# Performance work log

Measured on AMD Instinct MI355X. Metric: run time of the kernel, lower is better.

## Reference

```python
import jax, jax.numpy as jnp
import numpy as np

B, S, D, H = 4, 2048, 2048, 16
HD = D // H  # head_dim = 128


def setup_inputs() -> dict:
    key = jax.random.key(0)
    ks = jax.random.split(key, 9)
    s = 1.0 / np.sqrt(D)
    return {
        "x": jax.random.normal(ks[0], (B, S, D), dtype=jnp.float32),
        "wq": jax.random.normal(ks[1], (D, D), dtype=jnp.float32) * s,
        "bq": jnp.zeros((D,), dtype=jnp.float32),
        "wk": jax.random.normal(ks[2], (D, D), dtype=jnp.float32) * s,
        "bk": jnp.zeros((D,), dtype=jnp.float32),
        "wv": jax.random.normal(ks[3], (D, D), dtype=jnp.float32) * s,
        "bv": jnp.zeros((D,), dtype=jnp.float32),
        "wo": jax.random.normal(ks[4], (D, D), dtype=jnp.float32) * s,
        "bo": jnp.zeros((D,), dtype=jnp.float32),
    }


def reference(x, wq, bq, wk, bk, wv, bv, wo, bo):
    scale = HD ** -0.5
    # projections: [B,S,D] -> [B,S,H,HD] -> [B,H,S,HD]
    def split_heads(t):
        return t.reshape(B, S, H, HD).transpose(0, 2, 1, 3)
    q = split_heads(x @ wq + bq)
    k = split_heads(x @ wk + bk)
    v = split_heads(x @ wv + bv)
    scores = jnp.einsum('bhqd,bhkd->bhqk', q, k) * scale  # [B,H,S,S]
    attn = jax.nn.softmax(scores, axis=-1)
    out = jnp.einsum('bhqk,bhkd->bhqd', attn, v)  # [B,H,S,HD]
    out = out.transpose(0, 2, 1, 3).reshape(B, S, D)
    return out @ wo + bo
```

## Files before the change

kernel.cpp:

```cpp
#include <hip/hip_runtime.h>
#include <hip/hip_bf16.h>


typedef __attribute__((ext_vector_type(8))) short short8;
typedef __attribute__((ext_vector_type(4))) float floatx4;

#define DEV __device__ __forceinline__

DEV short f2bf(float f) {
    __hip_bfloat16 h = __float2bfloat16(f);
    return *reinterpret_cast<short*>(&h);
}

DEV void load_lds16(const __hip_bfloat16* g, short* l) {
    __builtin_amdgcn_global_load_lds(
        (const __attribute__((address_space(1))) void*)g,
        (__attribute__((address_space(3))) void*)l, 16, 0, 0);
}

__global__ void cast_x_kernel(const float* __restrict__ in,
                              __hip_bfloat16* __restrict__ out, int n8) {
    int i = blockIdx.x * 256 + threadIdx.x;
    if (i >= n8) return;
    const float4* p = reinterpret_cast<const float4*>(in) + (size_t)i * 2;
    float4 a = p[0], b = p[1];
    short8 r;
    r[0] = f2bf(a.x); r[1] = f2bf(a.y); r[2] = f2bf(a.z); r[3] = f2bf(a.w);
    r[4] = f2bf(b.x); r[5] = f2bf(b.y); r[6] = f2bf(b.z); r[7] = f2bf(b.w);
    *reinterpret_cast<short8*>(reinterpret_cast<short*>(out) + (size_t)i * 8) = r;
}

__global__ void transpose_cast_kernel(const float* __restrict__ wq,
                                      const float* __restrict__ wk,
                                      const float* __restrict__ wv,
                                      const float* __restrict__ wo,
                                      short* __restrict__ wt) {
    __shared__ float tile[32][33];
    const int z = blockIdx.z;
    const float* src = (z == 0) ? wq : (z == 1) ? wk : (z == 2) ? wv : wo;
    short* dst = wt + (size_t)z * 2048 * 2048;
    const int tx = threadIdx.x, ty = threadIdx.y;
    const int bx = blockIdx.x, by = blockIdx.y;
#pragma unroll
    for (int j = 0; j < 4; ++j)
        tile[ty + j * 8][tx] = src[(size_t)(by * 32 + ty + j * 8) * 2048 + bx * 32 + tx];
    __syncthreads();
#pragma unroll
    for (int j = 0; j < 4; ++j) {
        int r = ty + j * 8;
        dst[(size_t)(bx * 32 + r) * 2048 + by * 32 + tx] = f2bf(tile[tx][r]);
    }
}

template<int MODE>
__launch_bounds__(256, 2)
__global__ void gemm_bt_kernel(const __hip_bfloat16* __restrict__ A,
                               const __hip_bfloat16* __restrict__ Bt,
                               const float* __restrict__ bias0,
                               const float* __restrict__ bias1,
                               const float* __restrict__ bias2,
                               short* __restrict__ qbuf,
                               short* __restrict__ kbuf,
                               short* __restrict__ vtbuf,
                               float* __restrict__ outf) {
    constexpr int K = 2048;
    __shared__ short As[128 * 64];
    __shared__ short Bs[128 * 64];
    const int t = threadIdx.x, lane = t & 63, wid = t >> 6;
    const int lr = lane & 15, lg = lane >> 4;
    const int n0 = blockIdx.x * 128, m0 = blockIdx.y * 128;
    const int wm = (wid & 1) * 64, wn = (wid >> 1) * 64;

    floatx4 acc[4][4];
#pragma unroll
    for (int i = 0; i < 4; ++i)
#pragma unroll
        for (int j = 0; j < 4; ++j) acc[i][j] = (floatx4){0.f, 0.f, 0.f, 0.f};

    for (int kt = 0; kt < K / 64; ++kt) {
        __syncthreads();
#pragma unroll
        for (int i = 0; i < 4; ++i) {
            int fc = i * 256 + t;
            int row = fc >> 3, p = fc & 7;
            int col = (p ^ (row & 7)) << 3;
            load_lds16(A + (size_t)(m0 + row) * K + kt * 64 + col,
                       &As[(i * 256 + wid * 64) * 8]);
        }
#pragma unroll
        for (int i = 0; i < 4; ++i) {
            int fc = i * 256 + t;
            int row = fc >> 3, p = fc & 7;
            int col = (p ^ (row & 7)) << 3;
            load_lds16(Bt + (size_t)(n0 + row) * K + kt * 64 + col,
                       &Bs[(i * 256 + wid * 64) * 8]);
        }
        __syncthreads();
#pragma unroll
        for (int kk = 0; kk < 2; ++kk) {
            short8 af[4], bfr[4];
#pragma unroll
            for (int mi = 0; mi < 4; ++mi) {
                int row = wm + mi * 16 + lr;
                int c = lg + kk * 4;
                af[mi] = *(const short8*)&As[row * 64 + ((c ^ (row & 7)) << 3)];
            }
#pragma unroll
            for (int ni = 0; ni < 4; ++ni) {
                int row = wn + ni * 16 + lr;
                int c = lg + kk * 4;
                bfr[ni] = *(const short8*)&Bs[row * 64 + ((c ^ (row & 7)) << 3)];
            }
#pragma unroll
            for (int mi = 0; mi < 4; ++mi)
#pragma unroll
                for (int ni = 0; ni < 4; ++ni)
                    acc[mi][ni] = __builtin_amdgcn_mfma_f32_16x16x32_bf16(
                        af[mi], bfr[ni], acc[mi][ni], 0, 0, 0);
        }
    }

#pragma unroll
    for (int ni = 0; ni < 4; ++ni) {
        int n = n0 + wn + ni * 16 + lr;
        if (MODE == 0) {
            int which = n >> 11, d = n & 2047, h = d >> 7, hd = d & 127;
            const float* bias = (which == 0) ? bias0 : (which == 1) ? bias1 : bias2;
            float bval = bias[d];
            short* buf = (which == 0) ? qbuf : (which == 1) ? kbuf : vtbuf;
#pragma unroll
            for (int mi = 0; mi < 4; ++mi) {
                int m = m0 + wm + mi * 16 + lg * 4;
                int b = m >> 11, s = m & 2047;
                int bh = b * 16 + h;
#pragma unroll
                for (int r = 0; r < 4; ++r) {
                    float v = acc[mi][ni][r] + bval;
                    if (which < 2)
                        buf[((size_t)bh * 2048 + s + r) * 128 + hd] = f2bf(v);
                    else
                        buf[((size_t)bh * 128 + hd) * 2048 + s + r] = f2bf(v);
                }
            }
        } else {
            float bval = bias0[n];
#pragma unroll
            for (int mi = 0; mi < 4; ++mi) {
                int m = m0 + wm + mi * 16 + lg * 4;
#pragma unroll
                for (int r = 0; r < 4; ++r)
                    outf[(size_t)(m + r) * 2048 + n] = acc[mi][ni][r] + bval;
            }
        }
    }
}

__launch_bounds__(256, 2)
__global__ void attn_kernel(const __hip_bfloat16* __restrict__ qb,
                            const __hip_bfloat16* __restrict__ kb,
                            const __hip_bfloat16* __restrict__ vtb,
                            short* __restrict__ ob) {
    __shared__ short Ks[64 * 128];
    __shared__ short Vts[128 * 64];
    __shared__ short Ps[4][32 * 64];
    const int t = threadIdx.x, lane = t & 63, w = t >> 6;
    const int lr = lane & 15, lg = lane >> 4;
    const int bh = blockIdx.y, b = bh >> 4, h = bh & 15;
    const int q0 = blockIdx.x * 128;
    const __hip_bfloat16* qB = qb + (size_t)bh * 2048 * 128;
    const __hip_bfloat16* kB = kb + (size_t)bh * 2048 * 128;
    const __hip_bfloat16* vB = vtb + (size_t)bh * 128 * 2048;

    short8 aq[2][4];
#pragma unroll
    for (int mi = 0; mi < 2; ++mi) {
        int row = q0 + w * 32 + mi * 16 + lr;
#pragma unroll
        for (int kk = 0; kk < 4; ++kk)
            aq[mi][kk] = *(const short8*)(qB + (size_t)row * 128 + lg * 8 + kk * 32);
    }

    floatx4 o[2][8];
    float mv[2][4], lv[2][4];
#pragma unroll
    for (int mi = 0; mi < 2; ++mi) {
#pragma unroll
        for (int n = 0; n < 8; ++n) o[mi][n] = (floatx4){0.f, 0.f, 0.f, 0.f};
#pragma unroll
        for (int r = 0; r < 4; ++r) { mv[mi][r] = -1e30f; lv[mi][r] = 0.f; }
    }
    const float scale = 0.08838834764831845f;

    for (int kv = 0; kv < 32; ++kv) {
        __syncthreads();
#pragma unroll
        for (int i = 0; i < 4; ++i) {
            int fc = i * 256 + t, row = fc >> 4, p = fc & 15;
            load_lds16(kB + (size_t)(kv * 64 + row) * 128 + ((p ^ (row & 15)) << 3),
                       &Ks[(i * 256 + w * 64) * 8]);
        }
#pragma unroll
        for (int i = 0; i < 4; ++i) {
            int fc = i * 256 + t, row = fc >> 3, p = fc & 7;
            load_lds16(vB + (size_t)row * 2048 + kv * 64 + ((p ^ (row & 7)) << 3),
                       &Vts[(i * 256 + w * 64) * 8]);
        }
        __syncthreads();

#pragma unroll
        for (int mi = 0; mi < 2; ++mi) {
            floatx4 sfr[4];
#pragma unroll
            for (int tt = 0; tt < 4; ++tt) {
                floatx4 a = {0.f, 0.f, 0.f, 0.f};
#pragma unroll
                for (int kk = 0; kk < 4; ++kk) {
                    int row = tt * 16 + lr;
                    int c = lg + kk * 4;
                    short8 bk = *(const short8*)&Ks[row * 128 + ((c ^ (row & 15)) << 3)];
                    a = __builtin_amdgcn_mfma_f32_16x16x32_bf16(aq[mi][kk], bk, a, 0, 0, 0);
                }
                sfr[tt] = a * scale;
            }
#pragma unroll
            for (int r = 0; r < 4; ++r) {
                float pm = fmaxf(fmaxf(sfr[0][r], sfr[1][r]), fmaxf(sfr[2][r], sfr[3][r]));
                pm = fmaxf(pm, __shfl_xor(pm, 1));
                pm = fmaxf(pm, __shfl_xor(pm, 2));
                pm = fmaxf(pm, __shfl_xor(pm, 4));
                pm = fmaxf(pm, __shfl_xor(pm, 8));
                float mn = fmaxf(mv[mi][r], pm);
                float alpha = __expf(mv[mi][r] - mn);
                mv[mi][r] = mn;
                float ls = 0.f;
#pragma unroll
                for (int tt = 0; tt < 4; ++tt) {
                    float p = __expf(sfr[tt][r] - mn);
                    sfr[tt][r] = p;
                    ls += p;
                }
                ls += __shfl_xor(ls, 1);
                ls += __shfl_xor(ls, 2);
                ls += __shfl_xor(ls, 4);
                ls += __shfl_xor(ls, 8);
                lv[mi][r] = lv[mi][r] * alpha + ls;
#pragma unroll
                for (int n = 0; n < 8; ++n) o[mi][n][r] *= alpha;
            }
#pragma unroll
            for (int tt = 0; tt < 4; ++tt)
#pragma unroll
                for (int r = 0; r < 4; ++r) {
                    int row = mi * 16 + lg * 4 + r;
                    int cc = tt * 2 + (lr >> 3);
                    Ps[w][row * 64 + ((cc ^ (row & 7)) << 3) + (lane & 7)] =
                        f2bf(sfr[tt][r]);
                }
        }
#pragma unroll
        for (int mi = 0; mi < 2; ++mi) {
            short8 pa[2];
#pragma unroll
            for (int kk = 0; kk < 2; ++kk) {
                int row = mi * 16 + lr;
                int c = lg + kk * 4;
                pa[kk] = *(const short8*)&Ps[w][row * 64 + ((c ^ (row & 7)) << 3)];
            }
#pragma unroll
            for (int n = 0; n < 8; ++n) {
#pragma unroll
                for (int kk = 0; kk < 2; ++kk) {
                    int vrow = n * 16 + lr;
                    int c = lg + kk * 4;
                    short8 bv = *(const short8*)&Vts[vrow * 64 + ((c ^ (vrow & 7)) << 3)];
                    o[mi][n] = __builtin_amdgcn_mfma_f32_16x16x32_bf16(pa[kk], bv, o[mi][n], 0, 0, 0);
                }
            }
        }
    }

#pragma unroll
    for (int mi = 0; mi < 2; ++mi)
#pragma unroll
        for (int r = 0; r < 4; ++r) {
            float inv = 1.f / lv[mi][r];
            int srow = q0 + w * 32 + mi * 16 + lg * 4 + r;
            size_t base = ((size_t)b * 2048 + srow) * 2048 + h * 128;
#pragma unroll
            for (int n = 0; n < 8; ++n)
                ob[base + n * 16 + lr] = f2bf(o[mi][n][r] * inv);
        }
}

extern "C" void kernel_launch(void* const* d_in, const int* in_sizes, int n_in,
                              void* d_out, int out_size, void* d_ws, size_t ws_size,
                              hipStream_t stream) {
    (void)in_sizes; (void)n_in; (void)out_size; (void)ws_size;
    const float* x  = (const float*)d_in[0];
    const float* wq = (const float*)d_in[1];
    const float* bq = (const float*)d_in[2];
    const float* wk = (const float*)d_in[3];
    const float* bk = (const float*)d_in[4];
    const float* wv = (const float*)d_in[5];
    const float* bv = (const float*)d_in[6];
    const float* wo = (const float*)d_in[7];
    const float* bo = (const float*)d_in[8];
    float* out = (float*)d_out;

    char* ws = (char*)d_ws;
    const size_t SZ = (size_t)33554432;
    __hip_bfloat16* xbf = (__hip_bfloat16*)(ws);
    short* wt    = (short*)(ws + SZ);
    short* qbuf  = (short*)(ws + 2 * SZ);
    short* kbuf  = (short*)(ws + 3 * SZ);
    short* vtbuf = (short*)(ws + 4 * SZ);
    short* obuf  = (short*)(ws);

    cast_x_kernel<<<8192, 256, 0, stream>>>(x, xbf, 2097152);
    transpose_cast_kernel<<<dim3(64, 64, 4), dim3(32, 8), 0, stream>>>(wq, wk, wv, wo, wt);
    gemm_bt_kernel<0><<<dim3(48, 64), 256, 0, stream>>>(
        xbf, (const __hip_bfloat16*)wt, bq, bk, bv, qbuf, kbuf, vtbuf, nullptr);
    attn_kernel<<<dim3(16, 64), 256, 0, stream>>>(
        (const __hip_bfloat16*)qbuf, (const __hip_bfloat16*)kbuf,
        (const __hip_bfloat16*)vtbuf, obuf);
    gemm_bt_kernel<1><<<dim3(16, 64), 256, 0, stream>>>(
        (const __hip_bfloat16*)obuf, (const __hip_bfloat16*)(wt + (size_t)6144 * 2048),
        bo, nullptr, nullptr, nullptr, nullptr, nullptr, out);
}
```

Before: 757.2 us.

## Double-buffer K/V in attention, transpose MFMA operands, lazy softmax rescale

The attention kernel now double-buffers the K and V^T tiles in LDS, so the next tile's global-to-LDS load overlaps the current tile's compute, with one barrier per iteration. MFMA operands are swapped so each lane owns a single query row. That removes the cross-lane row reductions and allows packed bf16 conversion with vector LDS and output stores. The softmax scale is folded into the Q projection epilogue, and the running max is only updated when it grows by more than 8, skipping most rescales. Block IDs are remapped so blocks sharing a head land on the same XCD for L2 reuse, and s_setprio wraps the MFMA sections; the trade is twice the LDS, which may lower occupancy.

```diff
diff --git a/kernel.cpp b/kernel.cpp
--- a/kernel.cpp
+++ b/kernel.cpp
@@ -3,7 +3,9 @@
 
 
 typedef __attribute__((ext_vector_type(8))) short short8;
+typedef __attribute__((ext_vector_type(4))) short short4v;
 typedef __attribute__((ext_vector_type(4))) float floatx4;
+typedef unsigned int u32;
 
 #define DEV __device__ __forceinline__
 
@@ -16,6 +18,12 @@
     __builtin_amdgcn_global_load_lds(
         (const __attribute__((address_space(1))) void*)g,
         (__attribute__((address_space(3))) void*)l, 16, 0, 0);
+}
+
+DEV u32 cvt_pk_bf16(float lo, float hi) {
+    u32 r;
+    asm("v_cvt_pk_bf16_f32 %0, %1, %2" : "=v"(r) : "v"(lo), "v"(hi));
+    return r;
 }
 
 __global__ void cast_x_kernel(const float* __restrict__ in,
@@ -136,6 +144,7 @@
 #pragma unroll
                 for (int r = 0; r < 4; ++r) {
                     float v = acc[mi][ni][r] + bval;
+                    if (which == 0) v *= 0.08838834764831845f;
                     if (which < 2)
                         buf[((size_t)bh * 2048 + s + r) * 128 + hd] = f2bf(v);
                     else
@@ -160,13 +169,20 @@
                             const __hip_bfloat16* __restrict__ kb,
                             const __hip_bfloat16* __restrict__ vtb,
                             short* __restrict__ ob) {
-    __shared__ short Ks[64 * 128];
-    __shared__ short Vts[128 * 64];
-    __shared__ short Ps[4][32 * 64];
+    __shared__ short Ks[2][64 * 128];
+    __shared__ short Vts[2][128 * 64];
+    __shared__ short Pt[4][32 * 64];
+
     const int t = threadIdx.x, lane = t & 63, w = t >> 6;
     const int lr = lane & 15, lg = lane >> 4;
-    const int bh = blockIdx.y, b = bh >> 4, h = bh & 15;
-    const int q0 = blockIdx.x * 128;
+
+    int id = blockIdx.y * 16 + blockIdx.x;
+    int xcd = id & 7, slot = id >> 3;
+    int bh = xcd * 8 + (slot >> 4);
+    int qblk = slot & 15;
+    const int b = bh >> 4, h = bh & 15;
+    const int q0 = qblk * 128;
+
     const __hip_bfloat16* qB = qb + (size_t)bh * 2048 * 128;
     const __hip_bfloat16* kB = kb + (size_t)bh * 2048 * 128;
     const __hip_bfloat16* vB = vtb + (size_t)bh * 128 * 2048;
@@ -181,115 +197,135 @@
     }
 
     floatx4 o[2][8];
-    float mv[2][4], lv[2][4];
+    float mv[2], lv[2];
 #pragma unroll
     for (int mi = 0; mi < 2; ++mi) {
 #pragma unroll
         for (int n = 0; n < 8; ++n) o[mi][n] = (floatx4){0.f, 0.f, 0.f, 0.f};
-#pragma unroll
-        for (int r = 0; r < 4; ++r) { mv[mi][r] = -1e30f; lv[mi][r] = 0.f; }
-    }
-    const float scale = 0.08838834764831845f;
-
-    for (int kv = 0; kv < 32; ++kv) {
-        __syncthreads();
+        mv[mi] = -1e30f; lv[mi] = 0.f;
+    }
+
+    auto STAGE = [&](int d, int kv) {
 #pragma unroll
         for (int i = 0; i < 4; ++i) {
             int fc = i * 256 + t, row = fc >> 4, p = fc & 15;
             load_lds16(kB + (size_t)(kv * 64 + row) * 128 + ((p ^ (row & 15)) << 3),
-                       &Ks[(i * 256 + w * 64) * 8]);
+                       &Ks[d][(i * 256 + w * 64) * 8]);
         }
 #pragma unroll
         for (int i = 0; i < 4; ++i) {
             int fc = i * 256 + t, row = fc >> 3, p = fc & 7;
             load_lds16(vB + (size_t)row * 2048 + kv * 64 + ((p ^ (row & 7)) << 3),
-                       &Vts[(i * 256 + w * 64) * 8]);
-        }
-        __syncthreads();
+                       &Vts[d][(i * 256 + w * 64) * 8]);
+        }
+    };
+
+    STAGE(0, 0);
+    asm volatile("s_waitcnt vmcnt(0)" ::: "memory");
+    __builtin_amdgcn_s_barrier();
+
+    int cur = 0;
+    for (int kv = 0; kv < 32; ++kv) {
+        if (kv < 31) STAGE(cur ^ 1, kv + 1);
+
+        floatx4 sfr[2][4];
+#pragma unroll
+        for (int mi = 0; mi < 2; ++mi)
+#pragma unroll
+            for (int tt = 0; tt < 4; ++tt) sfr[mi][tt] = (floatx4){0.f, 0.f, 0.f, 0.f};
+        __builtin_amdgcn_s_setprio(1);
+#pragma unroll
+        for (int tt = 0; tt < 4; ++tt)
+#pragma unroll
+            for (int kk = 0; kk < 4; ++kk) {
+                int row = tt * 16 + lr;
+                int c = lg + kk * 4;
+                short8 bk = *(const short8*)&Ks[cur][row * 128 + ((c ^ (row & 15)) << 3)];
+                sfr[0][tt] = __builtin_amdgcn_mfma_f32_16x16x32_bf16(bk, aq[0][kk], sfr[0][tt], 0, 0, 0);
+                sfr[1][tt] = __builtin_amdgcn_mfma_f32_16x16x32_bf16(bk, aq[1][kk], sfr[1][tt], 0, 0, 0);
+            }
+        __builtin_amdgcn_s_setprio(0);
 
 #pragma unroll
         for (int mi = 0; mi < 2; ++mi) {
-            floatx4 sfr[4];
+            float pm = sfr[mi][0][0];
+#pragma unroll
+            for (int tt = 0; tt < 4; ++tt)
+#pragma unroll
+                for (int r = 0; r < 4; ++r) pm = fmaxf(pm, sfr[mi][tt][r]);
+            pm = fmaxf(pm, __shfl_xor(pm, 16));
+            pm = fmaxf(pm, __shfl_xor(pm, 32));
+            if (!__all(pm - mv[mi] <= 8.f)) {
+                float mn = fmaxf(mv[mi], pm);
+                float alpha = __expf(mv[mi] - mn);
+                mv[mi] = mn;
+                lv[mi] *= alpha;
+#pragma unroll
+                for (int n = 0; n < 8; ++n) o[mi][n] *= alpha;
+            }
+            float m = mv[mi], ls = 0.f;
+            u32 pk[8];
 #pragma unroll
             for (int tt = 0; tt < 4; ++tt) {
-                floatx4 a = {0.f, 0.f, 0.f, 0.f};
-#pragma unroll
-                for (int kk = 0; kk < 4; ++kk) {
-                    int row = tt * 16 + lr;
-                    int c = lg + kk * 4;
-                    short8 bk = *(const short8*)&Ks[row * 128 + ((c ^ (row & 15)) << 3)];
-                    a = __builtin_amdgcn_mfma_f32_16x16x32_bf16(aq[mi][kk], bk, a, 0, 0, 0);
-                }
-                sfr[tt] = a * scale;
-            }
-#pragma unroll
-            for (int r = 0; r < 4; ++r) {
-                float pm = fmaxf(fmaxf(sfr[0][r], sfr[1][r]), fmaxf(sfr[2][r], sfr[3][r]));
-                pm = fmaxf(pm, __shfl_xor(pm, 1));
-                pm = fmaxf(pm, __shfl_xor(pm, 2));
-                pm = fmaxf(pm, __shfl_xor(pm, 4));
-                pm = fmaxf(pm, __shfl_xor(pm, 8));
-                float mn = fmaxf(mv[mi][r], pm);
-                float alpha = __expf(mv[mi][r] - mn);
-                mv[mi][r] = mn;
-                float ls = 0.f;
-#pragma unroll
-                for (int tt = 0; tt < 4; ++tt) {
-                    float p = __expf(sfr[tt][r] - mn);
-                    sfr[tt][r] = p;
-                    ls += p;
-                }
-                ls += __shfl_xor(ls, 1);
-                ls += __shfl_xor(ls, 2);
-                ls += __shfl_xor(ls, 4);
-                ls += __shfl_xor(ls, 8);
-                lv[mi][r] = lv[mi][r] * alpha + ls;
-#pragma unroll
-                for (int n = 0; n < 8; ++n) o[mi][n][r] *= alpha;
-            }
-#pragma unroll
-            for (int tt = 0; tt < 4; ++tt)
-#pragma unroll
-                for (int r = 0; r < 4; ++r) {
-                    int row = mi * 16 + lg * 4 + r;
-                    int cc = tt * 2 + (lr >> 3);
-                    Ps[w][row * 64 + ((cc ^ (row & 7)) << 3) + (lane & 7)] =
-                        f2bf(sfr[tt][r]);
-                }
-        }
-#pragma unroll
-        for (int mi = 0; mi < 2; ++mi) {
-            short8 pa[2];
+                float p0 = __expf(sfr[mi][tt][0] - m);
+                float p1 = __expf(sfr[mi][tt][1] - m);
+                float p2 = __expf(sfr[mi][tt][2] - m);
+                float p3 = __expf(sfr[mi][tt][3] - m);
+                ls += (p0 + p1) + (p2 + p3);
+                pk[tt * 2] = cvt_pk_bf16(p0, p1);
+                pk[tt * 2 + 1] = cvt_pk_bf16(p2, p3);
+            }
+            ls += __shfl_xor(ls, 16);
+            ls += __shfl_xor(ls, 32);
+            lv[mi] += ls;
+#pragma unroll
+            for (int tt = 0; tt < 4; ++tt) {
+                int hgran = tt * 2 + (lg >> 1);
+                int idx = (mi * 16 + lr) * 64 + ((hgran ^ (lr & 7)) * 8) + (lg & 1) * 4;
+                *(uint2*)&Pt[w][idx] = make_uint2(pk[tt * 2], pk[tt * 2 + 1]);
+            }
+        }
+
+        short8 pa[2][2];
+#pragma unroll
+        for (int mi = 0; mi < 2; ++mi)
 #pragma unroll
             for (int kk = 0; kk < 2; ++kk) {
-                int row = mi * 16 + lr;
+                int hgran = kk * 4 + lg;
+                int idx = (mi * 16 + lr) * 64 + ((hgran ^ (lr & 7)) * 8);
+                pa[mi][kk] = *(const short8*)&Pt[w][idx];
+            }
+        __builtin_amdgcn_s_setprio(1);
+#pragma unroll
+        for (int n = 0; n < 8; ++n)
+#pragma unroll
+            for (int kk = 0; kk < 2; ++kk) {
+                int vrow = n * 16 + lr;
                 int c = lg + kk * 4;
-                pa[kk] = *(const short8*)&Ps[w][row * 64 + ((c ^ (row & 7)) << 3)];
-            }
-#pragma unroll
-            for (int n = 0; n < 8; ++n) {
-#pragma unroll
-                for (int kk = 0; kk < 2; ++kk) {
-                    int vrow = n * 16 + lr;
-                    int c = lg + kk * 4;
-                    short8 bv = *(const short8*)&Vts[vrow * 64 + ((c ^ (vrow & 7)) << 3)];
-                    o[mi][n] = __builtin_amdgcn_mfma_f32_16x16x32_bf16(pa[kk], bv, o[mi][n], 0, 0, 0);
-                }
-            }
-        }
-    }
-
-#pragma unroll
-    for (int mi = 0; mi < 2; ++mi)
-#pragma unroll
-        for (int r = 0; r < 4; ++r) {
-            float inv = 1.f / lv[mi][r];
-            int srow = q0 + w * 32 + mi * 16 + lg * 4 + r;
-            size_t base = ((size_t)b * 2048 + srow) * 2048 + h * 128;
-#pragma unroll
-            for (int n = 0; n < 8; ++n)
-                ob[base + n * 16 + lr] = f2bf(o[mi][n][r] * inv);
-        }
+                short8 bv = *(const short8*)&Vts[cur][vrow * 64 + ((c ^ (vrow & 7)) << 3)];
+                o[0][n] = __builtin_amdgcn_mfma_f32_16x16x32_bf16(bv, pa[0][kk], o[0][n], 0, 0, 0);
+                o[1][n] = __builtin_amdgcn_mfma_f32_16x16x32_bf16(bv, pa[1][kk], o[1][n], 0, 0, 0);
+            }
+        __builtin_amdgcn_s_setprio(0);
+
+        asm volatile("s_waitcnt vmcnt(0)" ::: "memory");
+        __builtin_amdgcn_s_barrier();
+        cur ^= 1;
+    }
+
+#pragma unroll
+    for (int mi = 0; mi < 2; ++mi) {
+        float inv = 1.f / lv[mi];
+        int s = q0 + w * 32 + mi * 16 + lr;
+        size_t base = ((size_t)b * 2048 + s) * 2048 + h * 128;
+#pragma unroll
+        for (int n = 0; n < 8; ++n) {
+            short4v vv;
+#pragma unroll
+            for (int r = 0; r < 4; ++r) vv[r] = f2bf(o[mi][n][r] * inv);
+            *(short4v*)&ob[base + n * 16 + lg * 4] = vv;
+        }
+    }
 }
 
 extern "C" void kernel_launch(void* const* d_in, const int* in_sizes, int n_in,
```

Result: faster. 672.7 us (-11.2%).
